# Performance work log

Measured on AMD Instinct MI355X. Metric: run time of the kernel, lower is better.

Reference implementation:

```python
import jax, jax.numpy as jnp
from jax import lax
import numpy as np

K = 3  # kernel_size

def _hamming2d():
    return jnp.asarray(np.outer(np.hamming(K), np.hamming(K)), dtype=jnp.float32)

def setup_inputs() -> dict:
    key = jax.random.key(0)
    k1, k2, k3 = jax.random.split(key, 3)
    B, C, H, W = 4, 256, 256, 256
    comp = 64
    x = jax.random.normal(k1, (B, C, H, W), dtype=jnp.float32)
    # xavier_normal for 1x1 compressor: std = sqrt(2/(fan_in+fan_out))
    w_comp = jax.random.normal(k2, (comp, C), dtype=jnp.float32) * np.sqrt(2.0 / (C + comp))
    # kernel generator: normal std=0.001, zero bias (as in _init_weights)
    w_gen = jax.random.normal(k3, (K * K, comp, 3, 3), dtype=jnp.float32) * 0.001
    b_gen = jnp.zeros((K * K,), dtype=jnp.float32)
    return {"x": x, "w_comp": w_comp, "w_gen": w_gen, "b_gen": b_gen}

def reference(x, w_comp, w_gen, b_gen):
    B, C, H, W = x.shape
    KK = K * K
    # 1x1 channel compression (no bias)
    compressed = jnp.einsum('bchw,oc->bohw', x, w_comp)
    # 3x3 conv, padding=1, with bias -> raw kernel logits (B, KK, H, W)
    logits = lax.conv_general_dilated(
        compressed, w_gen, window_strides=(1, 1), padding='SAME',
        dimension_numbers=('NCHW', 'OIHW', 'NCHW')) + b_gen[None, :, None, None]
    # softmax over the KK kernel taps per spatial position
    kw = jax.nn.softmax(logits, axis=1)
    # NOTE: original uses .view (memory reinterpret), not permute: (B,KK,H,W) -> (B,H,W,K,K)
    kw = kw.reshape(B, H, W, K, K) * _hamming2d()
    kw = kw / (kw.sum(axis=(-1, -2), keepdims=True) + 1e-8)
    kw = jnp.transpose(kw, (0, 3, 4, 1, 2)).reshape(B, KK, H, W)
    # adaptive aggregation: reflect pad + per-tap weighted sum (avoids KK x blowup)
    pad = K // 2
    xp = jnp.pad(x, ((0, 0), (0, 0), (pad, pad), (pad, pad)), mode='reflect')
    agg = jnp.zeros_like(x)
    for i in range(K):
        for j in range(K):
            agg = agg + xp[:, :, i:i + H, j:j + W] * kw[:, i * K + j][:, None]
    highpass = x - agg
    return x + highpass  # use_residual=True
```

## Files before the change

### kernel.cpp

```cpp
#include <hip/hip_runtime.h>
#include <stdint.h>

#define Bd 4
#define Cd 256
#define Hd 256
#define Wd 256
#define HW 65536
#define CM 64
#define KK 9
#define CG 32


typedef __attribute__((ext_vector_type(8))) short bf16x8;
typedef __attribute__((ext_vector_type(4))) float f32x4;

__device__ __forceinline__ uint32_t f2bf1(float f) {
    uint32_t u = __float_as_uint(f);
    return (u + 0x7FFFu + ((u >> 16) & 1u)) >> 16;
}
__device__ __forceinline__ uint32_t pkbf(float lo, float hi) {
    return f2bf1(lo) | (f2bf1(hi) << 16);
}

union BF8 { uint32_t u[4]; bf16x8 v; };

__device__ __forceinline__ void loadB(const float* __restrict__ px, int ks,
                                      float (&buf)[2][8]) {
#pragma unroll
    for (int n = 0; n < 2; ++n)
#pragma unroll
        for (int j = 0; j < 8; ++j)
            buf[n][j] = px[(size_t)(ks * 32 + j) * HW + n * 16];
}

__device__ __forceinline__ void stepMFMA(const float (&buf)[2][8],
                                         const short (*ws)[256], int ks,
                                         int l15, int lhi, int l7,
                                         f32x4 (&acc)[4][2]) {
    BF8 bn[2];
#pragma unroll
    for (int n = 0; n < 2; ++n) {
        bn[n].u[0] = pkbf(buf[n][0], buf[n][1]);
        bn[n].u[1] = pkbf(buf[n][2], buf[n][3]);
        bn[n].u[2] = pkbf(buf[n][4], buf[n][5]);
        bn[n].u[3] = pkbf(buf[n][6], buf[n][7]);
    }
#pragma unroll
    for (int m = 0; m < 4; ++m) {
        int gg = ((ks << 2) + lhi) ^ l7;
        bf16x8 af = *(const bf16x8*)&ws[m * 16 + l15][gg << 3];
        acc[m][0] = __builtin_amdgcn_mfma_f32_16x16x32_bf16(af, bn[0].v, acc[m][0], 0, 0, 0);
        acc[m][1] = __builtin_amdgcn_mfma_f32_16x16x32_bf16(af, bn[1].v, acc[m][1], 0, 0, 0);
    }
}

__global__ __launch_bounds__(256, 2) void compress_kernel(
    const float* __restrict__ x, const float* __restrict__ w_comp,
    float* __restrict__ comp)
{
    __shared__ short ws[CM][256];

    int tid = threadIdx.x;
    {
        int o  = tid >> 2;
        int k0 = (tid & 3) << 6;
        const float* wr = w_comp + o * Cd + k0;
        int xr = o & 7;
#pragma unroll
        for (int gi = 0; gi < 8; ++gi) {
            float4 a = *(const float4*)(wr + gi * 8);
            float4 c = *(const float4*)(wr + gi * 8 + 4);
            BF8 g;
            g.u[0] = pkbf(a.x, a.y); g.u[1] = pkbf(a.z, a.w);
            g.u[2] = pkbf(c.x, c.y); g.u[3] = pkbf(c.z, c.w);
            int gg = ((k0 >> 3) + gi) ^ xr;
            *(bf16x8*)&ws[o][gg << 3] = g.v;
        }
    }
    __syncthreads();

    int lane = tid & 63;
    int wv   = tid >> 6;
    int blk  = blockIdx.x;
    int b    = blk >> 9;
    int s0   = ((blk & 511) << 7) + (wv << 5);
    int l15  = lane & 15, lhi = lane >> 4, l7 = lane & 7;

    const float* px = x + (size_t)b * Cd * HW + (size_t)(lhi * 8) * HW + s0 + l15;

    f32x4 acc[4][2];
    f32x4 zz = {0.f, 0.f, 0.f, 0.f};
#pragma unroll
    for (int m = 0; m < 4; ++m)
#pragma unroll
        for (int n = 0; n < 2; ++n) acc[m][n] = zz;

    float pa[2][8], pb[2][8];
    loadB(px, 0, pa);
    for (int ks = 0; ks < 8; ks += 2) {
        loadB(px, ks + 1, pb);
        stepMFMA(pa, ws, ks, l15, lhi, l7, acc);
        if (ks + 2 < 8) loadB(px, ks + 2, pa);
        stepMFMA(pb, ws, ks + 1, l15, lhi, l7, acc);
    }

    float* ob = comp + (size_t)b * CM * HW + s0 + l15;
#pragma unroll
    for (int m = 0; m < 4; ++m)
#pragma unroll
        for (int n = 0; n < 2; ++n)
#pragma unroll
            for (int r = 0; r < 4; ++r)
                ob[(size_t)(m * 16 + lhi * 4 + r) * HW + n * 16] = acc[m][n][r];
}

__global__ __launch_bounds__(256) void kwgen_kernel(
    const float* __restrict__ comp, const float* __restrict__ w_gen,
    const float* __restrict__ b_gen, float* __restrict__ kw)
{
    __shared__ float wlds[CM][KK][12];
    for (int i = threadIdx.x; i < KK * CM * 9; i += 256) {
        int t = i / (CM * 9);
        int r = i - t * (CM * 9);
        int c = r / 9;
        int p = r - c * 9;
        wlds[c][t][p] = w_gen[i];
    }
    __syncthreads();

    int lane = threadIdx.x & 63;
    int q    = threadIdx.x >> 6;
    int b    = blockIdx.x >> 8;
    int h    = blockIdx.x & 255;
    int w    = q * 64 + lane;
    bool hmv = h > 0, hpv = h < Hd - 1;

    float acc[KK];
#pragma unroll
    for (int t = 0; t < KK; ++t) acc[t] = b_gen[t];

    const float* cb = comp + (size_t)b * CM * HW + h * Wd;
    for (int c = 0; c < CM; ++c) {
        const float* row = cb + (size_t)c * HW;
        float xm = hmv ? row[w - Wd] : 0.f;
        float xc = row[w];
        float xp = hpv ? row[w + Wd] : 0.f;
        float Lm = __shfl_up(xm, 1), Lc = __shfl_up(xc, 1), Lp = __shfl_up(xp, 1);
        float Rm = __shfl_down(xm, 1), Rc = __shfl_down(xc, 1), Rp = __shfl_down(xp, 1);
        if (lane == 0) {
            if (w == 0) { Lm = 0.f; Lc = 0.f; Lp = 0.f; }
            else {
                Lm = hmv ? row[w - 1 - Wd] : 0.f;
                Lc = row[w - 1];
                Lp = hpv ? row[w - 1 + Wd] : 0.f;
            }
        }
        if (lane == 63) {
            if (w == Wd - 1) { Rm = 0.f; Rc = 0.f; Rp = 0.f; }
            else {
                Rm = hmv ? row[w + 1 - Wd] : 0.f;
                Rc = row[w + 1];
                Rp = hpv ? row[w + 1 + Wd] : 0.f;
            }
        }
        float nb[9] = {Lm, xm, Rm, Lc, xc, Rc, Lp, xp, Rp};
#pragma unroll
        for (int t = 0; t < KK; ++t) {
            const float* wt = &wlds[c][t][0];
#pragma unroll
            for (int p = 0; p < 9; ++p)
                acc[t] = fmaf(nb[p], wt[p], acc[t]);
        }
    }
    float m = acc[0];
#pragma unroll
    for (int t = 1; t < KK; ++t) m = fmaxf(m, acc[t]);
    float sum = 0.f;
#pragma unroll
    for (int t = 0; t < KK; ++t) { acc[t] = __expf(acc[t] - m); sum += acc[t]; }
    float inv = 1.f / sum;
    int s = h * Wd + w;
    float* ob = kw + (size_t)b * KK * HW + s;
#pragma unroll
    for (int t = 0; t < KK; ++t) ob[(size_t)t * HW] = acc[t] * inv;
}

__global__ __launch_bounds__(256) void agg_kernel(
    const float* __restrict__ x, const float* __restrict__ kw,
    float* __restrict__ out)
{
    const float HAM[9] = {0.0064f, 0.08f, 0.0064f,
                          0.08f,   1.0f,  0.08f,
                          0.0064f, 0.08f, 0.0064f};
    int lane = threadIdx.x & 63;
    int wid  = threadIdx.x >> 6;
    int blk  = blockIdx.x;
    int h4 = blk & 63;
    int cg = (blk >> 6) & 7;
    int b  = blk >> 9;
    int h  = h4 * 4 + wid;
    int hm = (h == 0) ? 1 : h - 1;
    int hp = (h == Hd - 1) ? Hd - 2 : h + 1;

    float wv[4][9];
    {
        const float4* kv = (const float4*)(kw + (size_t)b * KK * HW
                                              + (size_t)h * (Wd * 9) + lane * 36);
        float t[36];
#pragma unroll
        for (int i = 0; i < 9; ++i) {
            float4 v = kv[i];
            t[i * 4 + 0] = v.x; t[i * 4 + 1] = v.y;
            t[i * 4 + 2] = v.z; t[i * 4 + 3] = v.w;
        }
#pragma unroll
        for (int j = 0; j < 4; ++j) {
            float s = 1e-8f;
#pragma unroll
            for (int p = 0; p < 9; ++p) { float u = t[j * 9 + p] * HAM[p]; wv[j][p] = u; s += u; }
            float inv = 1.f / s;
#pragma unroll
            for (int p = 0; p < 9; ++p) wv[j][p] *= inv;
        }
    }

    const float* xb = x + (size_t)b * Cd * HW;
    float* ob = out + (size_t)b * Cd * HW;
    int c0 = cg * CG;
    for (int c = c0; c < c0 + CG; ++c) {
        const float* xc0 = xb + (size_t)c * HW;
        float4 am = ((const float4*)(xc0 + hm * Wd))[lane];
        float4 ac = ((const float4*)(xc0 + h  * Wd))[lane];
        float4 ap = ((const float4*)(xc0 + hp * Wd))[lane];
        float Lm = __shfl_up(am.w, 1), Lc = __shfl_up(ac.w, 1), Lp = __shfl_up(ap.w, 1);
        float Rm = __shfl_down(am.x, 1), Rc = __shfl_down(ac.x, 1), Rp = __shfl_down(ap.x, 1);
        if (lane == 0)  { Lm = am.y; Lc = ac.y; Lp = ap.y; }
        if (lane == 63) { Rm = am.z; Rc = ac.z; Rp = ap.z; }
        float em[6] = {Lm, am.x, am.y, am.z, am.w, Rm};
        float ec[6] = {Lc, ac.x, ac.y, ac.z, ac.w, Rc};
        float ep[6] = {Lp, ap.x, ap.y, ap.z, ap.w, Rp};
        float o4[4];
#pragma unroll
        for (int j = 0; j < 4; ++j) {
            float agg = em[j] * wv[j][0];
            agg = fmaf(em[j + 1], wv[j][1], agg);
            agg = fmaf(em[j + 2], wv[j][2], agg);
            agg = fmaf(ec[j],     wv[j][3], agg);
            agg = fmaf(ec[j + 1], wv[j][4], agg);
            agg = fmaf(ec[j + 2], wv[j][5], agg);
            agg = fmaf(ep[j],     wv[j][6], agg);
            agg = fmaf(ep[j + 1], wv[j][7], agg);
            agg = fmaf(ep[j + 2], wv[j][8], agg);
            o4[j] = 2.f * ec[j + 1] - agg;
        }
        float4 o = {o4[0], o4[1], o4[2], o4[3]};
        ((float4*)(ob + (size_t)c * HW + h * Wd))[lane] = o;
    }
}

extern "C" void kernel_launch(void* const* d_in, const int* in_sizes, int n_in,
                              void* d_out, int out_size, void* d_ws, size_t ws_size,
                              hipStream_t stream) {
    const float* x      = (const float*)d_in[0];
    const float* w_comp = (const float*)d_in[1];
    const float* w_gen  = (const float*)d_in[2];
    const float* b_gen  = (const float*)d_in[3];
    float* out  = (float*)d_out;
    float* comp = (float*)d_ws;
    float* kw   = comp + (size_t)Bd * CM * HW;

    compress_kernel<<<2048, 256, 0, stream>>>(x, w_comp, comp);
    kwgen_kernel<<<1024, 256, 0, stream>>>(comp, w_gen, b_gen, kw);
    agg_kernel<<<2048, 256, 0, stream>>>(x, kw, out);
}
```

Baseline: 299.4 us.

## Stage x tiles through swizzled LDS with float4 loads in compress kernel

```diff
diff --git a/kernel.cpp b/kernel.cpp
--- a/kernel.cpp
+++ b/kernel.cpp
@@ -24,41 +24,12 @@
 
 union BF8 { uint32_t u[4]; bf16x8 v; };
 
-__device__ __forceinline__ void loadB(const float* __restrict__ px, int ks,
-                                      float (&buf)[2][8]) {
-#pragma unroll
-    for (int n = 0; n < 2; ++n)
-#pragma unroll
-        for (int j = 0; j < 8; ++j)
-            buf[n][j] = px[(size_t)(ks * 32 + j) * HW + n * 16];
-}
-
-__device__ __forceinline__ void stepMFMA(const float (&buf)[2][8],
-                                         const short (*ws)[256], int ks,
-                                         int l15, int lhi, int l7,
-                                         f32x4 (&acc)[4][2]) {
-    BF8 bn[2];
-#pragma unroll
-    for (int n = 0; n < 2; ++n) {
-        bn[n].u[0] = pkbf(buf[n][0], buf[n][1]);
-        bn[n].u[1] = pkbf(buf[n][2], buf[n][3]);
-        bn[n].u[2] = pkbf(buf[n][4], buf[n][5]);
-        bn[n].u[3] = pkbf(buf[n][6], buf[n][7]);
-    }
-#pragma unroll
-    for (int m = 0; m < 4; ++m) {
-        int gg = ((ks << 2) + lhi) ^ l7;
-        bf16x8 af = *(const bf16x8*)&ws[m * 16 + l15][gg << 3];
-        acc[m][0] = __builtin_amdgcn_mfma_f32_16x16x32_bf16(af, bn[0].v, acc[m][0], 0, 0, 0);
-        acc[m][1] = __builtin_amdgcn_mfma_f32_16x16x32_bf16(af, bn[1].v, acc[m][1], 0, 0, 0);
-    }
-}
-
-__global__ __launch_bounds__(256, 2) void compress_kernel(
+__global__ __launch_bounds__(256, 3) void compress_kernel(
     const float* __restrict__ x, const float* __restrict__ w_comp,
     float* __restrict__ comp)
 {
     __shared__ short ws[CM][256];
+    __shared__ float xs[32][128];
 
     int tid = threadIdx.x;
     {
@@ -77,16 +48,30 @@
             *(bf16x8*)&ws[o][gg << 3] = g.v;
         }
     }
-    __syncthreads();
 
     int lane = tid & 63;
     int wv   = tid >> 6;
     int blk  = blockIdx.x;
     int b    = blk >> 9;
-    int s0   = ((blk & 511) << 7) + (wv << 5);
+    int s0   = (blk & 511) << 7;
     int l15  = lane & 15, lhi = lane >> 4, l7 = lane & 7;
 
-    const float* px = x + (size_t)b * Cd * HW + (size_t)(lhi * 8) * HW + s0 + l15;
+    int sr   = tid >> 3;
+    int q    = sr & 7;
+    int sseg = (tid & 7) << 4;
+    int wflip = (sr >> 3) & 1;
+    const float* xrow = x + (size_t)b * Cd * HW + s0 + sseg;
+
+    float4 st[4];
+#pragma unroll
+    for (int i = 0; i < 4; ++i)
+        st[i] = *(const float4*)(xrow + (size_t)sr * HW + i * 4);
+#pragma unroll
+    for (int i = 0; i < 4; ++i) {
+        int pc = ((sseg + (i << 2)) ^ (wflip << 4)) ^ (q << 2);
+        *(float4*)&xs[sr][pc] = st[i];
+    }
+    __syncthreads();
 
     f32x4 acc[4][2];
     f32x4 zz = {0.f, 0.f, 0.f, 0.f};
@@ -95,23 +80,56 @@
 #pragma unroll
         for (int n = 0; n < 2; ++n) acc[m][n] = zz;
 
-    float pa[2][8], pb[2][8];
-    loadB(px, 0, pa);
-    for (int ks = 0; ks < 8; ks += 2) {
-        loadB(px, ks + 1, pb);
-        stepMFMA(pa, ws, ks, l15, lhi, l7, acc);
-        if (ks + 2 < 8) loadB(px, ks + 2, pa);
-        stepMFMA(pb, ws, ks + 1, l15, lhi, l7, acc);
-    }
-
-    float* ob = comp + (size_t)b * CM * HW + s0 + l15;
+    int rb   = lhi << 3;
+    int csw  = (lhi & 1) << 4;
+
+    for (int kc = 0; kc < 8; ++kc) {
+        if (kc < 7) {
+#pragma unroll
+            for (int i = 0; i < 4; ++i)
+                st[i] = *(const float4*)(xrow + (size_t)((kc + 1) * 32 + sr) * HW + i * 4);
+        }
+        BF8 bn[2];
+#pragma unroll
+        for (int n = 0; n < 2; ++n) {
+            int colb = (wv << 5) + (n << 4) + l15;
+            float e0 = xs[rb + 0][(colb ^ csw) ^ 0];
+            float e1 = xs[rb + 1][(colb ^ csw) ^ 4];
+            float e2 = xs[rb + 2][(colb ^ csw) ^ 8];
+            float e3 = xs[rb + 3][(colb ^ csw) ^ 12];
+            float e4 = xs[rb + 4][(colb ^ csw) ^ 16];
+            float e5 = xs[rb + 5][(colb ^ csw) ^ 20];
+            float e6 = xs[rb + 6][(colb ^ csw) ^ 24];
+            float e7 = xs[rb + 7][(colb ^ csw) ^ 28];
+            bn[n].u[0] = pkbf(e0, e1); bn[n].u[1] = pkbf(e2, e3);
+            bn[n].u[2] = pkbf(e4, e5); bn[n].u[3] = pkbf(e6, e7);
+        }
+#pragma unroll
+        for (int m = 0; m < 4; ++m) {
+            int gg = ((kc << 2) + lhi) ^ l7;
+            bf16x8 af = *(const bf16x8*)&ws[m * 16 + l15][gg << 3];
+            acc[m][0] = __builtin_amdgcn_mfma_f32_16x16x32_bf16(af, bn[0].v, acc[m][0], 0, 0, 0);
+            acc[m][1] = __builtin_amdgcn_mfma_f32_16x16x32_bf16(af, bn[1].v, acc[m][1], 0, 0, 0);
+        }
+        if (kc < 7) {
+            __syncthreads();
+#pragma unroll
+            for (int i = 0; i < 4; ++i) {
+                int pc = ((sseg + (i << 2)) ^ (wflip << 4)) ^ (q << 2);
+                *(float4*)&xs[sr][pc] = st[i];
+            }
+            __syncthreads();
+        }
+    }
+
+    float* ob = comp + (size_t)b * CM * HW + s0 + (wv << 5) + l15;
 #pragma unroll
     for (int m = 0; m < 4; ++m)
 #pragma unroll
         for (int n = 0; n < 2; ++n)
 #pragma unroll
             for (int r = 0; r < 4; ++r)
-                ob[(size_t)(m * 16 + lhi * 4 + r) * HW + n * 16] = acc[m][n][r];
+                ob[(size_t)(m * 16 + (lhi << 2) + r) * HW + n * 16] = acc[m][n][r];
 }
 
 __global__ __launch_bounds__(256) void kwgen_kernel(
```

Measured after the change: 340.0 us. +13.5%, slower.
